# Kernel tuning notes

Measured on AMD Instinct MI355X. Metric: run time of the kernel, lower is better.

## Reference

```python
import jax, jax.numpy as jnp
import numpy as np
import math

B, T, E, H = 4, 1024, 1024, 16
HD = E // H  # 64, even -> rope_dim == head_dim, no pass-through
SCALE = HD ** -0.5
PI = math.pi


def setup_inputs() -> dict:
    key = jax.random.key(0)
    ks = jax.random.split(key, 16)
    d = {}
    d["x_real"] = jax.random.normal(ks[0], (B, T, E), jnp.float32)
    d["x_imag"] = jax.random.normal(ks[1], (B, T, E), jnp.float32)
    d["lat"] = jax.random.uniform(ks[2], (B, T), jnp.float32) * 180.0
    d["lon"] = jax.random.uniform(ks[3], (B, T), jnp.float32) * 360.0
    i = 4
    for p in ("q", "k", "v", "o"):
        d[p + "_log_mag"] = jax.random.normal(ks[i], (E, E), jnp.float32) * 0.1; i += 1
        d[p + "_phase"] = jax.random.uniform(ks[i], (E, E), jnp.float32, minval=-PI, maxval=PI); i += 1
        d[p + "_bmag"] = jnp.zeros((E,), jnp.float32)
        d[p + "_bphase"] = jnp.zeros((E,), jnp.float32)
    d["dist_scale"] = jax.random.normal(ks[i], (H,), jnp.float32) * 0.1 - 0.5; i += 1
    d["dist_offset"] = jnp.zeros((H,), jnp.float32)
    return d


def _clinear(xr, xi, log_mag, phase, bmag, bphase):
    # Complex linear with magnitude-phase weights: W = exp(log_mag) * e^{i*phase}
    mag = jnp.exp(log_mag)
    wr = mag * jnp.cos(phase)
    wi = mag * jnp.sin(phase)
    r = xr @ wr.T - xi @ wi.T + bmag * jnp.cos(bphase)
    im = xr @ wi.T + xi @ wr.T + bmag * jnp.sin(bphase)
    return r, im


def _rotate_half(x):
    x1, x2 = jnp.split(x, 2, axis=-1)
    return jnp.concatenate([-x2, x1], axis=-1)


def _rope(xr, xi, cos_full, sin_full):
    # applied identically to real and imag parts (head_dim even -> full rope)
    r = xr * cos_full + _rotate_half(xr) * sin_full
    im = xi * cos_full + _rotate_half(xi) * sin_full
    return r, im


def _heads(x):  # [B,T,E] -> [B,H,T,HD]
    return x.reshape(B, T, H, HD).transpose(0, 2, 1, 3)


def _forward(x_real, x_imag, lat, lon,
             q_log_mag, q_phase, q_bmag, q_bphase,
             k_log_mag, k_phase, k_bmag, k_bphase,
             v_log_mag, v_phase, v_bmag, v_bphase,
             o_log_mag, o_phase, o_bmag, o_bphase,
             dist_scale, dist_offset):
    qr, qi = _clinear(x_real, x_imag, q_log_mag, q_phase, q_bmag, q_bphase)
    kr, ki = _clinear(x_real, x_imag, k_log_mag, k_phase, k_bmag, k_bphase)
    vr, vi = _clinear(x_real, x_imag, v_log_mag, v_phase, v_bmag, v_bphase)
    qr, qi, kr, ki, vr, vi = map(_heads, (qr, qi, kr, ki, vr, vi))

    # complex RoPE cache
    pos = jnp.arange(T, dtype=jnp.float32)
    inv_freq = 1.0 / (10000.0 ** (jnp.arange(0, HD, 2, dtype=jnp.float32) / HD))
    freqs = pos[:, None] * inv_freq[None, :]          # [T, HD/2]
    cos = jnp.cos(freqs); sin = jnp.sin(freqs)
    cos_full = jnp.concatenate([cos, cos], -1)[None, None]  # [1,1,T,HD]
    sin_full = jnp.concatenate([sin, sin], -1)[None, None]
    qr, qi = _rope(qr, qi, cos_full, sin_full)
    kr, ki = _rope(kr, ki, cos_full, sin_full)

    # Hermitian attention scores: Re(Q K^H) = Re(Q)Re(K)^T + Im(Q)Im(K)^T
    scores = (jnp.einsum('bhqd,bhkd->bhqk', qr, kr)
              + jnp.einsum('bhqd,bhkd->bhqk', qi, ki)) * SCALE

    # spatial attention bias via haversine distance
    lat_rad = (lat - 90.0) / 180.0 * PI
    lon_rad = lon / 360.0 * (2.0 * PI)
    lat1 = lat_rad[:, :, None]; lat2 = lat_rad[:, None, :]   # [B,T,1],[B,1,T]
    dlat = lat2 - lat1
    dlon = lon_rad[:, None, :] - lon_rad[:, :, None]
    a = jnp.sin(dlat / 2) ** 2 + jnp.cos(lat1) * jnp.cos(lat2) * jnp.sin(dlon / 2) ** 2
    dist_deg = 2.0 * jnp.arcsin(jnp.sqrt(jnp.clip(a, 0.0, 1.0))) * (180.0 / PI)
    log_dist = jnp.log1p(dist_deg)[:, None]                  # [B,1,T,T]
    bias = dist_scale[None, :, None, None] * log_dist + dist_offset[None, :, None, None]
    scores = scores + bias

    # causal mask (block_size == T)
    causal = jnp.tril(jnp.ones((T, T), dtype=bool))
    scores = jnp.where(causal[None, None], scores, jnp.float32(-1e9))
    attn = jax.nn.softmax(scores, axis=-1)

    # complex value aggregation: real attention weights times complex V
    or_ = jnp.einsum('bhqk,bhkd->bhqd', attn, vr)
    oi_ = jnp.einsum('bhqk,bhkd->bhqd', attn, vi)
    or_ = or_.transpose(0, 2, 1, 3).reshape(B, T, E)
    oi_ = oi_.transpose(0, 2, 1, 3).reshape(B, T, E)

    yr, yi = _clinear(or_, oi_, o_log_mag, o_phase, o_bmag, o_bphase)
    return jnp.stack([yr, yi])  # [2,B,T,E] (real, imag)


def reference(x_real, x_imag, lat, lon,
              q_log_mag, q_phase, q_bmag, q_bphase,
              k_log_mag, k_phase, k_bmag, k_bphase,
              v_log_mag, v_phase, v_bmag, v_bphase,
              o_log_mag, o_phase, o_bmag, o_bphase,
              dist_scale, dist_offset):
    return _forward(x_real, x_imag, lat, lon,
                    q_log_mag, q_phase, q_bmag, q_bphase,
                    k_log_mag, k_phase, k_bmag, k_bphase,
                    v_log_mag, v_phase, v_bmag, v_bphase,
                    o_log_mag, o_phase, o_bmag, o_bphase,
                    dist_scale, dist_offset)
```

## Files before the change

kernel.cpp:

```cpp
#include <hip/hip_runtime.h>
#include <math.h>

#define B_ 4
#define T_ 1024
#define E_ 1024
#define H_ 16
#define HD_ 64

constexpr float SCALE_ = 0.125f;
constexpr float PI_F = 3.14159265358979323846f;

constexpr size_t BTE = (size_t)B_ * T_ * E_;
constexpr size_t BTT = (size_t)B_ * T_ * T_;
constexpr int M_ = B_ * T_;
constexpr int KC_ = 2 * E_;

typedef __attribute__((ext_vector_type(8))) short bf16x8;
typedef __attribute__((ext_vector_type(4))) float f32x4;

__device__ __forceinline__ short f2bf(float f) {
    unsigned int u = __float_as_uint(f);
    unsigned int r = (u + 0x7fffu + ((u >> 16) & 1u)) >> 16;
    return (short)r;
}
__device__ __forceinline__ float bf2f(short s) {
    return __uint_as_float(((unsigned int)(unsigned short)s) << 16);
}
__device__ __forceinline__ void fsplit(float v, short& h, short& l) {
    short hh = f2bf(v);
    h = hh;
    l = f2bf(v - bf2f(hh));
}
__device__ __forceinline__ void gl_lds16(const void* g, void* l) {
    __builtin_amdgcn_global_load_lds(
        (const __attribute__((address_space(1))) unsigned int*)g,
        (__attribute__((address_space(3))) unsigned int*)l, 16, 0, 0);
}

__global__ __launch_bounds__(256) void wgen(const float* __restrict__ lm,
                                            const float* __restrict__ ph,
                                            short* __restrict__ W) {
    int idx = blockIdx.x * 256 + threadIdx.x;
    int n = idx >> 10, k = idx & 1023;
    float m = expf(lm[idx]);
    float s, c;
    sincosf(ph[idx], &s, &c);
    float wr = m * c, wi = m * s;
    size_t r0 = (size_t)n * KC_;
    size_t r1 = (size_t)(n + 1024) * KC_;
    W[r0 + k]        = f2bf(wr);
    W[r0 + 1024 + k] = f2bf(-wi);
    W[r1 + k]        = f2bf(wi);
    W[r1 + 1024 + k] = f2bf(wr);
}

__global__ __launch_bounds__(256) void wgen_split(const float* __restrict__ lm,
                                                  const float* __restrict__ ph,
                                                  short* __restrict__ Wh,
                                                  short* __restrict__ Wl) {
    int idx = blockIdx.x * 256 + threadIdx.x;
    int n = idx >> 10, k = idx & 1023;
    float m = expf(lm[idx]);
    float s, c;
    sincosf(ph[idx], &s, &c);
    float wr = m * c, wi = m * s;
    size_t o0 = (size_t)n * KC_ + k;
    size_t o1 = (size_t)n * KC_ + 1024 + k;
    size_t o2 = (size_t)(n + 1024) * KC_ + k;
    size_t o3 = (size_t)(n + 1024) * KC_ + 1024 + k;
    short h, l;
    fsplit(wr,  h, l); Wh[o0] = h; Wl[o0] = l;
    fsplit(-wi, h, l); Wh[o1] = h; Wl[o1] = l;
    fsplit(wi,  h, l); Wh[o2] = h; Wl[o2] = l;
    fsplit(wr,  h, l); Wh[o3] = h; Wl[o3] = l;
}

__global__ __launch_bounds__(256) void xcat_split(const float* __restrict__ xr,
                                                  const float* __restrict__ xi,
                                                  short* __restrict__ xh,
                                                  short* __restrict__ xl) {
    size_t idx = (size_t)blockIdx.x * 256 + threadIdx.x;
    size_t m = idx >> 10, k = idx & 1023;
    short h, l;
    fsplit(xr[idx], h, l);
    xh[m * KC_ + k] = h; xl[m * KC_ + k] = l;
    fsplit(xi[idx], h, l);
    xh[m * KC_ + 1024 + k] = h; xl[m * KC_ + 1024 + k] = l;
}

__global__ __launch_bounds__(256) void geodist(const float* __restrict__ lat,
                                               const float* __restrict__ lon,
                                               short* __restrict__ ld) {
    size_t idx = (size_t)blockIdx.x * 256 + threadIdx.x;
    int k = (int)(idx & (T_ - 1));
    int q = (int)((idx >> 10) & (T_ - 1));
    int b = (int)(idx >> 20);
    float la1 = (lat[b * T_ + q] - 90.f) * (PI_F / 180.f);
    float la2 = (lat[b * T_ + k] - 90.f) * (PI_F / 180.f);
    float lo1 = lon[b * T_ + q] * (PI_F / 180.f);
    float lo2 = lon[b * T_ + k] * (PI_F / 180.f);
    float sdla = sinf((la2 - la1) * 0.5f);
    float sdlo = sinf((lo2 - lo1) * 0.5f);
    float a = sdla * sdla + cosf(la1) * cosf(la2) * sdlo * sdlo;
    a = fminf(fmaxf(a, 0.f), 1.f);
    float dd = 2.f * asinf(sqrtf(a)) * (180.f / PI_F);
    ld[idx] = f2bf(log1pf(dd));
}

__global__ __launch_bounds__(512, 2) void cgemm_qk2(const short* __restrict__ Ah,
                                                    const short* __restrict__ Al,
                                                    const short* __restrict__ Qwh,
                                                    const short* __restrict__ Qwl,
                                                    const short* __restrict__ Kwh,
                                                    const short* __restrict__ Kwl,
                                                    const float* __restrict__ qbm,
                                                    const float* __restrict__ qbp,
                                                    const float* __restrict__ kbm,
                                                    const float* __restrict__ kbp,
                                                    short* __restrict__ Qh,
                                                    short* __restrict__ Ql,
                                                    short* __restrict__ Kh,
                                                    short* __restrict__ Kl) {
    __shared__ short lds[2][4096 * 8];

    const int tid = threadIdx.x;
    const int w = tid >> 6, l = tid & 63;
    const int wm = w >> 1;
    const int wn = w & 1;
    const int wl = l & 15, g = l >> 4;

    const int id = blockIdx.x;
    const int x = id & 7;
    const int j = id >> 3;
    const int bm = ((x & 3) * 4 + (j & 3)) * 256;
    const int bnc = ((x >> 2) * 8 + (j >> 2)) * 128;

    f32x4 accQ[4][4], accK[4][4];
#pragma unroll
    for (int m = 0; m < 4; ++m)
#pragma unroll
        for (int n = 0; n < 4; ++n) {
            accQ[m][n] = (f32x4){0.f, 0.f, 0.f, 0.f};
            accK[m][n] = (f32x4){0.f, 0.f, 0.f, 0.f};
        }

    auto stage = [&](int k0, int buf) {
#pragma unroll
        for (int i = 0; i < 8; ++i) {
            const int c = i * 512 + tid;
            short* dst = &lds[buf][(size_t)c * 8];
            if (c < 2048) {
                const int row = c >> 3, c8 = (c & 7) ^ (row & 7);
                gl_lds16(((c8 < 4) ? Ah : Al) + (size_t)(bm + row) * KC_ + k0 + (c8 & 3) * 8, dst);
            } else if (c < 3072) {
                const int lc = c - 2048, row = lc >> 3, c8 = (lc & 7) ^ (row & 7);
                gl_lds16(((c8 < 4) ? Qwh : Qwl) + (size_t)(bnc + row) * KC_ + k0 + (c8 & 3) * 8, dst);
            } else {
                const int lc = c - 3072, row = lc >> 3, c8 = (lc & 7) ^ (row & 7);
                gl_lds16(((c8 < 4) ? Kwh : Kwl) + (size_t)(bnc + row) * KC_ + k0 + (c8 & 3) * 8, dst);
            }
        }
    };

    const int NT = KC_ / 32;
    stage(0, 0);
    __syncthreads();

    int cur = 0;
    for (int t = 0; t < NT; ++t) {
        if (t + 1 < NT) stage((t + 1) * 32, cur ^ 1);

        const short* sA = &lds[cur][0];
        const short* sQ = &lds[cur][2048 * 8];
        const short* sK = &lds[cur][3072 * 8];

        bf16x8 afh[4], afl[4];
#pragma unroll
        for (int m = 0; m < 4; ++m) {
            const int ra = wm * 64 + m * 16 + wl;
            const int sw = ra & 7;
            afh[m] = *(const bf16x8*)&sA[(ra * 8 + (g ^ sw)) * 8];
            afl[m] = *(const bf16x8*)&sA[(ra * 8 + ((g + 4) ^ sw)) * 8];
        }
#pragma unroll
        for (int n = 0; n < 4; ++n) {
            const int rb = wn * 64 + n * 16 + wl;
            const int sw = rb & 7;
            const bf16x8 qh_ = *(const bf16x8*)&sQ[(rb * 8 + (g ^ sw)) * 8];
            const bf16x8 ql_ = *(const bf16x8*)&sQ[(rb * 8 + ((g + 4) ^ sw)) * 8];
            const bf16x8 kh_ = *(const bf16x8*)&sK[(rb * 8 + (g ^ sw)) * 8];
            const bf16x8 kl_ = *(const bf16x8*)&sK[(rb * 8 + ((g + 4) ^ sw)) * 8];
#pragma unroll
            for (int m = 0; m < 4; ++m) {
                accQ[m][n] = __builtin_amdgcn_mfma_f32_16x16x32_bf16(afh[m], qh_, accQ[m][n], 0, 0, 0);
                accQ[m][n] = __builtin_amdgcn_mfma_f32_16x16x32_bf16(afh[m], ql_, accQ[m][n], 0, 0, 0);
                accQ[m][n] = __builtin_amdgcn_mfma_f32_16x16x32_bf16(afl[m], qh_, accQ[m][n], 0, 0, 0);
                accK[m][n] = __builtin_amdgcn_mfma_f32_16x16x32_bf16(afh[m], kh_, accK[m][n], 0, 0, 0);
                accK[m][n] = __builtin_amdgcn_mfma_f32_16x16x32_bf16(afh[m], kl_, accK[m][n], 0, 0, 0);
                accK[m][n] = __builtin_amdgcn_mfma_f32_16x16x32_bf16(afl[m], kh_, accK[m][n], 0, 0, 0);
            }
        }
        __syncthreads();
        cur ^= 1;
    }

#pragma unroll
    for (int n = 0; n < 4; ++n) {
        const int col = bnc + wn * 64 + n * 16 + wl;
        const int ch = col & 1023;
        float qs, qc, ks, kc;
        sincosf(qbp[ch], &qs, &qc);
        sincosf(kbp[ch], &ks, &kc);
        const float qbias = qbm[ch] * (col < 1024 ? qc : qs);
        const float kbias = kbm[ch] * (col < 1024 ? kc : ks);
#pragma unroll
        for (int m = 0; m < 4; ++m)
#pragma unroll
            for (int r = 0; r < 4; ++r) {
                accQ[m][n][r] += qbias;
                accK[m][n][r] += kbias;
            }
    }

#pragma unroll
    for (int n = 0; n < 2; ++n) {
        const int jf = n * 16 + wl;
        const float invf = expf(-(2.f * jf / 64.f) * 9.210340371976184f);
#pragma unroll
        for (int m = 0; m < 4; ++m)
#pragma unroll
            for (int r = 0; r < 4; ++r) {
                const int row = bm + wm * 64 + m * 16 + g * 4 + r;
                const float th = (float)(row & 1023) * invf;
                float s_, c_;
                sincosf(th, &s_, &c_);
                float x1 = accQ[m][n][r], x2 = accQ[m][n + 2][r];
                accQ[m][n][r]     = x1 * c_ - x2 * s_;
                accQ[m][n + 2][r] = x2 * c_ + x1 * s_;
                x1 = accK[m][n][r]; x2 = accK[m][n + 2][r];
                accK[m][n][r]     = x1 * c_ - x2 * s_;
                accK[m][n + 2][r] = x2 * c_ + x1 * s_;
            }
    }

#pragma unroll
    for (int n = 0; n < 4; ++n) {
        const int col = bnc + wn * 64 + n * 16 + wl;
        const int ch = col & 1023;
        const int off = (ch >> 6) * 128 + (ch & 63) + ((col >= 1024) ? 64 : 0);
#pragma unroll
        for (int m = 0; m < 4; ++m)
#pragma unroll
            for (int r = 0; r < 4; ++r) {
                const int row = bm + wm * 64 + m * 16 + g * 4 + r;
                short h_, l_;
                fsplit(accQ[m][n][r], h_, l_);
                Qh[(size_t)row * KC_ + off] = h_;
                Ql[(size_t)row * KC_ + off] = l_;
                fsplit(accK[m][n][r], h_, l_);
                Kh[(size_t)row * KC_ + off] = h_;
                Kl[(size_t)row * KC_ + off] = l_;
            }
    }
}

__global__ __launch_bounds__(256) void cgemm_mfma(const short* __restrict__ A,
                                                  const short* __restrict__ W,
                                                  const float* __restrict__ bmag,
                                                  const float* __restrict__ bphase,
                                                  short* __restrict__ outbf,
                                                  float* __restrict__ outr,
                                                  float* __restrict__ outi,
                                                  int mode) {
    __shared__ short lds[2][1024 * 8];

    const int tid = threadIdx.x;
    const int w = tid >> 6, l = tid & 63;
    const int wm = w >> 1, wn = w & 1;
    const int wl = l & 15, g = l >> 4;

    int id = blockIdx.y * 32 + blockIdx.x;
    int swz = (id & 7) * 64 + (id >> 3);
    const int bm = (swz & 31) * 128;
    const int bn = (swz >> 5) * 128;

    f32x4 acc[4][4];
#pragma unroll
    for (int m = 0; m < 4; ++m)
#pragma unroll
        for (int n = 0; n < 4; ++n) acc[m][n] = (f32x4){0.f, 0.f, 0.f, 0.f};

    auto stage = [&](int k0, int buf) {
#pragma unroll
        for (int i = 0; i < 4; ++i) {
            const int c = i * 256 + tid;
            const int row = c >> 3, c8 = (c & 7) ^ (row & 7);
            const short* src = (c8 < 4)
                ? A + (size_t)(bm + row) * KC_ + k0 + (c8 & 3) * 8
                : W + (size_t)(bn + row) * KC_ + k0 + (c8 & 3) * 8;
            gl_lds16(src, &lds[buf][(size_t)c * 8]);
        }
    };

    const int NT = KC_ / 32;
    stage(0, 0);
    __syncthreads();

    int cur = 0;
    for (int t = 0; t < NT; ++t) {
        if (t + 1 < NT) stage((t + 1) * 32, cur ^ 1);

        const short* sAB = lds[cur];
        bf16x8 af[4], bfr[4];
#pragma unroll
        for (int m = 0; m < 4; ++m) {
            const int ra = wm * 64 + m * 16 + wl;
            af[m] = *(const bf16x8*)&sAB[(ra * 8 + (g ^ (ra & 7))) * 8];
        }
#pragma unroll
        for (int n = 0; n < 4; ++n) {
            const int rb = wn * 64 + n * 16 + wl;
            bfr[n] = *(const bf16x8*)&sAB[(rb * 8 + ((g + 4) ^ (rb & 7))) * 8];
        }
#pragma unroll
        for (int m = 0; m < 4; ++m)
#pragma unroll
            for (int n = 0; n < 4; ++n)
                acc[m][n] = __builtin_amdgcn_mfma_f32_16x16x32_bf16(af[m], bfr[n], acc[m][n], 0, 0, 0);

        __syncthreads();
        cur ^= 1;
    }

#pragma unroll
    for (int n = 0; n < 4; ++n) {
        const int col = bn + wn * 64 + n * 16 + wl;
        const int ch = col & 1023;
        float sb, cb;
        sincosf(bphase[ch], &sb, &cb);
        const float bias = bmag[ch] * (col < 1024 ? cb : sb);
#pragma unroll
        for (int m = 0; m < 4; ++m) {
#pragma unroll
            for (int r = 0; r < 4; ++r) {
                const int row = bm + wm * 64 + m * 16 + g * 4 + r;
                const float v = acc[m][n][r] + bias;
                if (mode == 0) {
                    const int hh = ch >> 6, d = ch & 63;
                    outbf[(size_t)row * KC_ + hh * 128 + d + ((col >= 1024) ? 64 : 0)] = f2bf(v);
                } else {
                    if (col < 1024) outr[(size_t)row * E_ + col] = v;
                    else            outi[(size_t)row * E_ + (col - 1024)] = v;
                }
            }
        }
    }
}

__global__ __launch_bounds__(512) void attn_split(const short* __restrict__ qh,
                                                  const short* __restrict__ ql,
                                                  const short* __restrict__ kh,
                                                  const short* __restrict__ kl,
                                                  const short* __restrict__ vc,
                                                  const short* __restrict__ ldb,
                                                  const float* __restrict__ dsc,
                                                  const float* __restrict__ dof,
                                                  short* __restrict__ otc) {
    __shared__ short sKh[64 * 128];
    __shared__ short sKl[64 * 128];
    __shared__ short sV[2][64 * 66];
    __shared__ short sP[8][16 * 68];

    const int j = blockIdx.x;
    const int h = j & 15;
    const int idx = j >> 4;
    const int b = idx & 3;
    const int q4 = idx >> 2;
    const int qt = (q4 < 4) ? (7 - q4) : (q4 - 4);

    const int tid = threadIdx.x;
    const int w = tid >> 6, l = tid & 63;
    const int wl = l & 15, g = l >> 4;

    const float dsch = dsc[h], dofh = dof[h];

    bf16x8 aqh[4], aql[4];
    {
        const size_t qbase = ((size_t)(b * T_) + qt * 128 + w * 16 + wl) * KC_ + h * 128;
#pragma unroll
        for (int ks = 0; ks < 4; ++ks) {
            aqh[ks] = *(const bf16x8*)(qh + qbase + ks * 32 + g * 8);
            aql[ks] = *(const bf16x8*)(ql + qbase + ks * 32 + g * 8);
        }
    }

    f32x4 accR[4], accI[4];
#pragma unroll
    for (int nb = 0; nb < 4; ++nb) {
        accR[nb] = (f32x4){0.f, 0.f, 0.f, 0.f};
        accI[nb] = (f32x4){0.f, 0.f, 0.f, 0.f};
    }
    float m_run[4], l_run[4];
#pragma unroll
    for (int r = 0; r < 4; ++r) { m_run[r] = -3.0e38f; l_run[r] = 0.f; }

    const int nkt = 2 * qt + 2;
    for (int kt = 0; kt < nkt; ++kt) {
        __syncthreads();

#pragma unroll
        for (int i = 0; i < 2; ++i) {
            int chunk = (w * 2 + i) * 64 + l;
            int row = chunk >> 4;
            int c8 = (chunk & 15) ^ (row & 15);
            size_t src = ((size_t)(b * T_) + kt * 64 + row) * KC_ + h * 128 + c8 * 8;
            gl_lds16(kh + src, sKh + (w * 2 + i) * 64 * 8);
            gl_lds16(kl + src, sKl + (w * 2 + i) * 64 * 8);
        }
        {
            const short* vrow = vc + ((size_t)(b * T_) + kt * 64 + l) * KC_ + h * 128;
            const int comp = w >> 2;
            const int d0 = (w & 3) * 16;
#pragma unroll
            for (int half = 0; half < 2; ++half) {
                bf16x8 v8 = *(const bf16x8*)(vrow + comp * 64 + d0 + half * 8);
#pragma unroll
                for (int jj = 0; jj < 8; ++jj) sV[comp][(d0 + half * 8 + jj) * 66 + l] = v8[jj];
            }
        }
        __syncthreads();

        f32x4 s[4];
#pragma unroll
        for (int nb = 0; nb < 4; ++nb) s[nb] = (f32x4){0.f, 0.f, 0.f, 0.f};
#pragma unroll
        for (int nb = 0; nb < 4; ++nb) {
            const int ktl = nb * 16 + wl;
#pragma unroll
            for (int ks = 0; ks < 4; ++ks) {
                const int pc8 = (ks * 4 + g) ^ (ktl & 15);
                const bf16x8 bkh = *(const bf16x8*)&sKh[ktl * 128 + pc8 * 8];
                const bf16x8 bkl = *(const bf16x8*)&sKl[ktl * 128 + pc8 * 8];
                s[nb] = __builtin_amdgcn_mfma_f32_16x16x32_bf16(aqh[ks], bkh, s[nb], 0, 0, 0);
                s[nb] = __builtin_amdgcn_mfma_f32_16x16x32_bf16(aqh[ks], bkl, s[nb], 0, 0, 0);
                s[nb] = __builtin_amdgcn_mfma_f32_16x16x32_bf16(aql[ks], bkh, s[nb], 0, 0, 0);
            }
        }

        const int qg0 = qt * 128 + w * 16 + g * 4;
        const int kg0 = kt * 64;
        const bool domask = (kt >= 2 * qt);
#pragma unroll
        for (int nb = 0; nb < 4; ++nb) {
            const int kg = kg0 + nb * 16 + wl;
            const short* ldp = ldb + ((size_t)b * T_ + qg0) * T_ + kg;
#pragma unroll
            for (int r = 0; r < 4; ++r) {
                float sv = s[nb][r] * SCALE_ + dsch * bf2f(ldp[(size_t)r * T_]) + dofh;
                if (domask && kg > qg0 + r) sv = -1.0e9f;
                s[nb][r] = sv;
            }
        }

#pragma unroll
        for (int r = 0; r < 4; ++r) {
            float mt = fmaxf(fmaxf(s[0][r], s[1][r]), fmaxf(s[2][r], s[3][r]));
            mt = fmaxf(mt, __shfl_xor(mt, 1));
            mt = fmaxf(mt, __shfl_xor(mt, 2));
            mt = fmaxf(mt, __shfl_xor(mt, 4));
            mt = fmaxf(mt, __shfl_xor(mt, 8));
            const float mnew = fmaxf(m_run[r], mt);
            const float sc = __expf(m_run[r] - mnew);
            m_run[r] = mnew;
            float rs = 0.f;
#pragma unroll
            for (int nb = 0; nb < 4; ++nb) {
                const float p = __expf(s[nb][r] - mnew);
                s[nb][r] = p;
                rs += p;
            }
            rs += __shfl_xor(rs, 1);
            rs += __shfl_xor(rs, 2);
            rs += __shfl_xor(rs, 4);
            rs += __shfl_xor(rs, 8);
            l_run[r] = l_run[r] * sc + rs;
#pragma unroll
            for (int nb = 0; nb < 4; ++nb) { accR[nb][r] *= sc; accI[nb][r] *= sc; }
        }

#pragma unroll
        for (int nb = 0; nb < 4; ++nb)
#pragma unroll
            for (int r = 0; r < 4; ++r)
                sP[w][(g * 4 + r) * 68 + nb * 16 + wl] = f2bf(s[nb][r]);

        bf16x8 ap[2];
#pragma unroll
        for (int ks = 0; ks < 2; ++ks)
            ap[ks] = *(const bf16x8*)&sP[w][wl * 68 + ks * 32 + g * 8];
#pragma unroll
        for (int nb = 0; nb < 4; ++nb) {
#pragma unroll
            for (int ks = 0; ks < 2; ++ks) {
                const bf16x8 bvr = *(const bf16x8*)&sV[0][(nb * 16 + wl) * 66 + ks * 32 + g * 8];
                const bf16x8 bvi = *(const bf16x8*)&sV[1][(nb * 16 + wl) * 66 + ks * 32 + g * 8];
                accR[nb] = __builtin_amdgcn_mfma_f32_16x16x32_bf16(ap[ks], bvr, accR[nb], 0, 0, 0);
                accI[nb] = __builtin_amdgcn_mfma_f32_16x16x32_bf16(ap[ks], bvi, accI[nb], 0, 0, 0);
            }
        }
    }

    float inv[4];
#pragma unroll
    for (int r = 0; r < 4; ++r) inv[r] = 1.0f / l_run[r];
#pragma unroll
    for (int nb = 0; nb < 4; ++nb) {
#pragma unroll
        for (int r = 0; r < 4; ++r) {
            const int q = qt * 128 + w * 16 + g * 4 + r;
            const int d = nb * 16 + wl;
            const size_t base = ((size_t)(b * T_) + q) * KC_ + h * 64 + d;
            otc[base] = f2bf(accR[nb][r] * inv[r]);
            otc[base + 1024] = f2bf(accI[nb][r] * inv[r]);
        }
    }
}

extern "C" void kernel_launch(void* const* d_in, const int* in_sizes, int n_in,
                              void* d_out, int out_size, void* d_ws, size_t ws_size,
                              hipStream_t stream) {
    const float* x_r  = (const float*)d_in[0];
    const float* x_i  = (const float*)d_in[1];
    const float* lat  = (const float*)d_in[2];
    const float* lon  = (const float*)d_in[3];
    const float* q_lm = (const float*)d_in[4];
    const float* q_ph = (const float*)d_in[5];
    const float* q_bm = (const float*)d_in[6];
    const float* q_bp = (const float*)d_in[7];
    const float* k_lm = (const float*)d_in[8];
    const float* k_ph = (const float*)d_in[9];
    const float* k_bm = (const float*)d_in[10];
    const float* k_bp = (const float*)d_in[11];
    const float* v_lm = (const float*)d_in[12];
    const float* v_ph = (const float*)d_in[13];
    const float* v_bm = (const float*)d_in[14];
    const float* v_bp = (const float*)d_in[15];
    const float* o_lm = (const float*)d_in[16];
    const float* o_ph = (const float*)d_in[17];
    const float* o_bm = (const float*)d_in[18];
    const float* o_bp = (const float*)d_in[19];
    const float* dsc  = (const float*)d_in[20];
    const float* dof  = (const float*)d_in[21];

    char* ws = (char*)d_ws;
    const size_t MB = 1024u * 1024u;
    short* Wv  = (short*)(ws + 0 * MB);
    short* Wo  = (short*)(ws + 8 * MB);
    short* Wqh = (short*)(ws + 16 * MB);
    short* Wql = (short*)(ws + 24 * MB);
    short* Wkh = (short*)(ws + 32 * MB);
    short* Wkl = (short*)(ws + 40 * MB);
    short* xch = (short*)(ws + 48 * MB);
    short* xcl = (short*)(ws + 64 * MB);
    short* qhh = (short*)(ws + 80 * MB);
    short* qll = (short*)(ws + 96 * MB);
    short* khh = (short*)(ws + 112 * MB);
    short* kll = (short*)(ws + 128 * MB);
    short* vcb = (short*)(ws + 144 * MB);
    short* otc = (short*)(ws + 160 * MB);
    short* ldt = (short*)(ws + 176 * MB);

    wgen_split<<<(E_ * E_) / 256, 256, 0, stream>>>(q_lm, q_ph, Wqh, Wql);
    wgen_split<<<(E_ * E_) / 256, 256, 0, stream>>>(k_lm, k_ph, Wkh, Wkl);
    wgen<<<(E_ * E_) / 256, 256, 0, stream>>>(v_lm, v_ph, Wv);
    wgen<<<(E_ * E_) / 256, 256, 0, stream>>>(o_lm, o_ph, Wo);
    xcat_split<<<BTE / 256, 256, 0, stream>>>(x_r, x_i, xch, xcl);
    geodist<<<BTT / 256, 256, 0, stream>>>(lat, lon, ldt);

    cgemm_qk2<<<256, 512, 0, stream>>>(xch, xcl, Wqh, Wql, Wkh, Wkl,
                                       q_bm, q_bp, k_bm, k_bp,
                                       qhh, qll, khh, kll);

    dim3 ggrid(M_ / 128, KC_ / 128);
    cgemm_mfma<<<ggrid, 256, 0, stream>>>(xch, Wv, v_bm, v_bp, vcb, nullptr, nullptr, 0);

    attn_split<<<512, 512, 0, stream>>>(qhh, qll, khh, kll, vcb, ldt, dsc, dof, otc);

    float* yr = (float*)d_out;
    float* yi = (float*)d_out + BTE;
    cgemm_mfma<<<ggrid, 256, 0, stream>>>(otc, Wo, o_bm, o_bp, nullptr, yr, yi, 1);
}
```

Before: 603.6 us.

## Merge four weight-generation launches into one and raise MFMA wave priority in attention

```diff
diff --git a/kernel.cpp b/kernel.cpp
--- a/kernel.cpp
+++ b/kernel.cpp
@@ -37,42 +37,41 @@
         (__attribute__((address_space(3))) unsigned int*)l, 16, 0, 0);
 }
 
-__global__ __launch_bounds__(256) void wgen(const float* __restrict__ lm,
-                                            const float* __restrict__ ph,
-                                            short* __restrict__ W) {
-    int idx = blockIdx.x * 256 + threadIdx.x;
-    int n = idx >> 10, k = idx & 1023;
+__global__ __launch_bounds__(256) void wgen_all(const float* __restrict__ qlm, const float* __restrict__ qph,
+                                                const float* __restrict__ klm, const float* __restrict__ kph,
+                                                const float* __restrict__ vlm, const float* __restrict__ vph,
+                                                const float* __restrict__ olm, const float* __restrict__ oph,
+                                                short* __restrict__ Wqh, short* __restrict__ Wql,
+                                                short* __restrict__ Wkh, short* __restrict__ Wkl,
+                                                short* __restrict__ Wv,  short* __restrict__ Wo) {
+    const int which = blockIdx.x >> 12;
+    const int idx = (blockIdx.x & 4095) * 256 + threadIdx.x;
+    const int n = idx >> 10, k = idx & 1023;
+    const float* lm = (which == 0) ? qlm : (which == 1) ? klm : (which == 2) ? vlm : olm;
+    const float* ph = (which == 0) ? qph : (which == 1) ? kph : (which == 2) ? vph : oph;
     float m = expf(lm[idx]);
     float s, c;
     sincosf(ph[idx], &s, &c);
-    float wr = m * c, wi = m * s;
-    size_t r0 = (size_t)n * KC_;
-    size_t r1 = (size_t)(n + 1024) * KC_;
-    W[r0 + k]        = f2bf(wr);
-    W[r0 + 1024 + k] = f2bf(-wi);
-    W[r1 + k]        = f2bf(wi);
-    W[r1 + 1024 + k] = f2bf(wr);
-}
-
-__global__ __launch_bounds__(256) void wgen_split(const float* __restrict__ lm,
-                                                  const float* __restrict__ ph,
-                                                  short* __restrict__ Wh,
-                                                  short* __restrict__ Wl) {
-    int idx = blockIdx.x * 256 + threadIdx.x;
-    int n = idx >> 10, k = idx & 1023;
-    float m = expf(lm[idx]);
-    float s, c;
-    sincosf(ph[idx], &s, &c);
-    float wr = m * c, wi = m * s;
-    size_t o0 = (size_t)n * KC_ + k;
-    size_t o1 = (size_t)n * KC_ + 1024 + k;
-    size_t o2 = (size_t)(n + 1024) * KC_ + k;
-    size_t o3 = (size_t)(n + 1024) * KC_ + 1024 + k;
-    short h, l;
-    fsplit(wr,  h, l); Wh[o0] = h; Wl[o0] = l;
-    fsplit(-wi, h, l); Wh[o1] = h; Wl[o1] = l;
-    fsplit(wi,  h, l); Wh[o2] = h; Wl[o2] = l;
-    fsplit(wr,  h, l); Wh[o3] = h; Wl[o3] = l;
+    const float wr = m * c, wi = m * s;
+    const size_t o0 = (size_t)n * KC_ + k;
+    const size_t o1 = (size_t)n * KC_ + 1024 + k;
+    const size_t o2 = (size_t)(n + 1024) * KC_ + k;
+    const size_t o3 = (size_t)(n + 1024) * KC_ + 1024 + k;
+    if (which < 2) {
+        short* Wh = which ? Wkh : Wqh;
+        short* Wl = which ? Wkl : Wql;
+        short h, l;
+        fsplit(wr,  h, l); Wh[o0] = h; Wl[o0] = l;
+        fsplit(-wi, h, l); Wh[o1] = h; Wl[o1] = l;
+        fsplit(wi,  h, l); Wh[o2] = h; Wl[o2] = l;
+        fsplit(wr,  h, l); Wh[o3] = h; Wl[o3] = l;
+    } else {
+        short* W = (which == 2) ? Wv : Wo;
+        W[o0] = f2bf(wr);
+        W[o1] = f2bf(-wi);
+        W[o2] = f2bf(wi);
+        W[o3] = f2bf(wr);
+    }
 }
 
 __global__ __launch_bounds__(256) void xcat_split(const float* __restrict__ xr,
@@ -433,6 +432,7 @@
         f32x4 s[4];
 #pragma unroll
         for (int nb = 0; nb < 4; ++nb) s[nb] = (f32x4){0.f, 0.f, 0.f, 0.f};
+        __builtin_amdgcn_s_setprio(1);
 #pragma unroll
         for (int nb = 0; nb < 4; ++nb) {
             const int ktl = nb * 16 + wl;
@@ -446,6 +446,7 @@
                 s[nb] = __builtin_amdgcn_mfma_f32_16x16x32_bf16(aql[ks], bkh, s[nb], 0, 0, 0);
             }
         }
+        __builtin_amdgcn_s_setprio(0);
 
         const int qg0 = qt * 128 + w * 16 + g * 4;
         const int kg0 = kt * 64;
@@ -498,6 +499,7 @@
 #pragma unroll
         for (int ks = 0; ks < 2; ++ks)
             ap[ks] = *(const bf16x8*)&sP[w][wl * 68 + ks * 32 + g * 8];
+        __builtin_amdgcn_s_setprio(1);
 #pragma unroll
         for (int nb = 0; nb < 4; ++nb) {
 #pragma unroll
@@ -508,6 +510,7 @@
                 accI[nb] = __builtin_amdgcn_mfma_f32_16x16x32_bf16(ap[ks], bvi, accI[nb], 0, 0, 0);
             }
         }
+        __builtin_amdgcn_s_setprio(0);
     }
 
     float inv[4];
@@ -570,10 +573,8 @@
     short* otc = (short*)(ws + 160 * MB);
     short* ldt = (short*)(ws + 176 * MB);
 
-    wgen_split<<<(E_ * E_) / 256, 256, 0, stream>>>(q_lm, q_ph, Wqh, Wql);
-    wgen_split<<<(E_ * E_) / 256, 256, 0, stream>>>(k_lm, k_ph, Wkh, Wkl);
-    wgen<<<(E_ * E_) / 256, 256, 0, stream>>>(v_lm, v_ph, Wv);
-    wgen<<<(E_ * E_) / 256, 256, 0, stream>>>(o_lm, o_ph, Wo);
+    wgen_all<<<4 * 4096, 256, 0, stream>>>(q_lm, q_ph, k_lm, k_ph, v_lm, v_ph, o_lm, o_ph,
+                                           Wqh, Wql, Wkh, Wkl, Wv, Wo);
     xcat_split<<<BTE / 256, 256, 0, stream>>>(x_r, x_i, xch, xcl);
     geodist<<<BTT / 256, 256, 0, stream>>>(lat, lon, ldt);
 
```

After: 591.8 us. About the same (-2.0%).
